# Optimization experiments

Measured on AMD Instinct MI355X. Metric: run time of the kernel, lower is better.

## Reference

```python
import jax, jax.numpy as jnp
import numpy as np

SEGMENT_LENGTHS = [2048, 4096, 8192]
DILATION_RATES = [1, 2, 4]
EPS = 1e-8


def setup_inputs() -> dict:
    key = jax.random.key(0)
    kq, kk, kv = jax.random.split(key, 3)
    shape = (4, 8192, 8, 64)  # (b, n, h, d)
    return {
        "query": jax.random.normal(kq, shape, dtype=jnp.float32),
        "key": jax.random.normal(kk, shape, dtype=jnp.float32),
        "value": jax.random.normal(kv, shape, dtype=jnp.float32),
    }


def _dilated_attention(query, key, value):
    b, n, h, d = query.shape
    ng = len(SEGMENT_LENGTHS)
    group_sizes = [h // ng] * ng
    for i in range(h % ng):
        group_sizes[i] += 1
    scale = 1.0 / (d ** 0.5)  # torch SDPA default: 1/sqrt(E), E = last dim

    out = jnp.zeros_like(query)
    for i, (g, r, s) in enumerate(zip(group_sizes, DILATION_RATES, SEGMENT_LENGTHS)):
        offset = i % r
        hmin = sum(group_sizes[:i])
        hmax = hmin + g
        nseg = n // s
        # (b, nseg, s, h, d) -> strided dilation slice + head-group slice
        qg = query.reshape(b, nseg, s, h, d)[:, :, offset::r, hmin:hmax, :]
        kg = key.reshape(b, nseg, s, h, d)[:, :, offset::r, hmin:hmax, :]
        vg = value.reshape(b, nseg, s, h, d)[:, :, offset::r, hmin:hmax, :]
        # Faithful to the torch code: SDPA is fed (bn, s, h, d) untransposed, so
        # attention is over the HEAD axis (length g); s is a batch-like axis.
        scores = jnp.einsum('bnsqd,bnskd->bnsqk', qg, kg) * scale  # (b,nseg,sd,g,g)
        attn = jax.nn.softmax(scores, axis=-1)
        x = jnp.einsum('bnsqk,bnskd->bnsqd', attn, vg)  # (b,nseg,sd,g,d)
        # custom sum-normalization over (segment, dilated-position) dims
        x = x / (x.sum(axis=(1, 2), keepdims=True) + EPS)
        # scatter-add back into the strided/head-sliced locations
        out = (out.reshape(b, nseg, s, h, d)
                  .at[:, :, offset::r, hmin:hmax, :].add(x)
                  .reshape(b, n, h, d))
    return out / ng


def reference(query, key, value):
    return _dilated_attention(query, key, value)
```

## Files before the change

### kernel.cpp

```cpp
#include <hip/hip_runtime.h>
#include <math.h>

#define NB 4
#define NN 8192
#define NH 8
#define ND 64
#define ROWF (NH * ND)
#define NPART_STRIDE 192
#define N_BLOCKS_P1 1792
#define N_WAVES_P1  (N_BLOCKS_P1 * 4)


__device__ __forceinline__ float dot4(float4 a, float4 b) {
    return a.x * b.x + a.y * b.y + a.z * b.z + a.w * b.w;
}

template<int HOFF>
__device__ __forceinline__ void pass1_g3(
    const float* __restrict__ Q, const float* __restrict__ K,
    const float* __restrict__ V, float* __restrict__ out,
    float* __restrict__ partials,
    int b, int cw, int wid, int r, int off, int seglen)
{
    const int lane = threadIdx.x & 63;
    const int sg   = lane >> 4;
    const int l15  = lane & 15;

    float xs0 = 0.f, xs1 = 0.f, xs2 = 0.f, xs3 = 0.f;

    #pragma unroll 2
    for (int t = 0; t < 8; ++t) {
        const int j   = cw * 8 + t;
        const int pos = (j >> 11) * seglen + off + (j & 2047) * r;
        const size_t rb = ((size_t)b * NN + pos) * ROWF;

        const float4 qv = *(const float4*)(Q + rb + HOFF + 4 * lane);
        const float4 k0 = *(const float4*)(K + rb + HOFF + 0 * ND + 4 * l15);
        const float4 k1 = *(const float4*)(K + rb + HOFF + 1 * ND + 4 * l15);
        const float4 k2 = *(const float4*)(K + rb + HOFF + 2 * ND + 4 * l15);
        const float4 v0 = *(const float4*)(V + rb + HOFF + 0 * ND + 4 * l15);
        const float4 v1 = *(const float4*)(V + rb + HOFF + 1 * ND + 4 * l15);
        const float4 v2 = *(const float4*)(V + rb + HOFF + 2 * ND + 4 * l15);

        float s0 = dot4(qv, k0), s1 = dot4(qv, k1), s2 = dot4(qv, k2);
        #pragma unroll
        for (int o = 8; o >= 1; o >>= 1) {
            s0 += __shfl_xor(s0, o);
            s1 += __shfl_xor(s1, o);
            s2 += __shfl_xor(s2, o);
        }

        s0 *= 0.125f; s1 *= 0.125f; s2 *= 0.125f;
        const float m  = fmaxf(s0, fmaxf(s1, s2));
        const float e0 = __expf(s0 - m), e1 = __expf(s1 - m), e2 = __expf(s2 - m);
        const float rs = 1.f / (e0 + e1 + e2);
        const float w0 = e0 * rs, w1 = e1 * rs, w2 = e2 * rs;

        const float xe0 = w0 * v0.x + w1 * v1.x + w2 * v2.x;
        const float xe1 = w0 * v0.y + w1 * v1.y + w2 * v2.y;
        const float xe2 = w0 * v0.z + w1 * v1.z + w2 * v2.z;
        const float xe3 = w0 * v0.w + w1 * v1.w + w2 * v2.w;

        if (sg < 3)
            *(float4*)(out + rb + HOFF + 4 * lane) = make_float4(xe0, xe1, xe2, xe3);
        xs0 += xe0; xs1 += xe1; xs2 += xe2; xs3 += xe3;
    }

    if (sg < 3)
        *(float4*)(partials + (size_t)wid * NPART_STRIDE + sg * 64 + 4 * l15) =
            make_float4(xs0, xs1, xs2, xs3);
}

__device__ __forceinline__ void pass1_g2(
    const float* __restrict__ Q, const float* __restrict__ K,
    const float* __restrict__ V, float* __restrict__ out,
    float* __restrict__ partials, int b, int cw, int wid)
{
    const int lane = threadIdx.x & 63;
    const int half = lane >> 5;
    const int sg2  = (lane >> 4) & 1;
    const int l15  = lane & 15;
    const int l31  = lane & 31;

    float xs0 = 0.f, xs1 = 0.f, xs2 = 0.f, xs3 = 0.f;

    #pragma unroll 2
    for (int t = 0; t < 4; ++t) {
        const int j   = cw * 8 + t * 2 + half;
        const int pos = 2 + 4 * j;
        const size_t rb = ((size_t)b * NN + pos) * ROWF + 384;

        const float4 qv = *(const float4*)(Q + rb + 4 * l31);
        const float4 k0 = *(const float4*)(K + rb + 0 * ND + 4 * l15);
        const float4 k1 = *(const float4*)(K + rb + 1 * ND + 4 * l15);
        const float4 v0 = *(const float4*)(V + rb + 0 * ND + 4 * l15);
        const float4 v1 = *(const float4*)(V + rb + 1 * ND + 4 * l15);

        float s0 = dot4(qv, k0), s1 = dot4(qv, k1);
        #pragma unroll
        for (int o = 8; o >= 1; o >>= 1) {
            s0 += __shfl_xor(s0, o);
            s1 += __shfl_xor(s1, o);
        }

        s0 *= 0.125f; s1 *= 0.125f;
        const float m  = fmaxf(s0, s1);
        const float e0 = __expf(s0 - m), e1 = __expf(s1 - m);
        const float rs = 1.f / (e0 + e1);
        const float w0 = e0 * rs, w1 = e1 * rs;

        const float xe0 = w0 * v0.x + w1 * v1.x;
        const float xe1 = w0 * v0.y + w1 * v1.y;
        const float xe2 = w0 * v0.z + w1 * v1.z;
        const float xe3 = w0 * v0.w + w1 * v1.w;

        *(float4*)(out + rb + 4 * l31) = make_float4(xe0, xe1, xe2, xe3);
        xs0 += xe0; xs1 += xe1; xs2 += xe2; xs3 += xe3;
    }

    xs0 += __shfl_xor(xs0, 32); xs1 += __shfl_xor(xs1, 32);
    xs2 += __shfl_xor(xs2, 32); xs3 += __shfl_xor(xs3, 32);
    if (half == 0)
        *(float4*)(partials + (size_t)wid * NPART_STRIDE + sg2 * 64 + 4 * l15) =
            make_float4(xs0, xs1, xs2, xs3);
}

__global__ __launch_bounds__(256)
void sda_pass1(const float* __restrict__ Q, const float* __restrict__ K,
               const float* __restrict__ V, float* __restrict__ out,
               float* __restrict__ partials)
{
    const int bid = blockIdx.x;
    const int w   = threadIdx.x >> 6;
    const int wid = bid * 4 + w;
    if (bid < 1024) {
        const int b = bid >> 8, cw = (bid & 255) * 4 + w;
        pass1_g3<0>(Q, K, V, out, partials, b, cw, wid, 1, 0, 2048);
    } else if (bid < 1536) {
        const int loc = bid - 1024;
        const int b = loc >> 7, cw = (loc & 127) * 4 + w;
        pass1_g3<192>(Q, K, V, out, partials, b, cw, wid, 2, 1, 4096);
    } else {
        const int loc = bid - 1536;
        const int b = loc >> 6, cw = (loc & 63) * 4 + w;
        pass1_g2(Q, K, V, out, partials, b, cw, wid);
    }
}

__global__ __launch_bounds__(256)
void sda_pass2a(const float* __restrict__ partials, float* __restrict__ partial2)
{
    const int bid   = blockIdx.x;
    const int bh    = bid >> 3;
    const int slice = bid & 7;
    const int b     = bh >> 3;
    const int h     = bh & 7;
    const int d     = threadIdx.x & 63;
    const int part  = threadIdx.x >> 6;
    int qi, wstart, cnt;
    if (h < 3)      { qi = h;     wstart = b * 1024;       cnt = 1024; }
    else if (h < 6) { qi = h - 3; wstart = 4096 + b * 512; cnt = 512;  }
    else            { qi = h - 6; wstart = 6144 + b * 256; cnt = 256;  }
    const int len = cnt >> 3;
    const int c0  = wstart + slice * len;
    float s = 0.f;
    #pragma unroll 4
    for (int c = part; c < len; c += 4)
        s += partials[(size_t)(c0 + c) * NPART_STRIDE + qi * 64 + d];
    __shared__ float sred[4][64];
    sred[part][d] = s;
    __syncthreads();
    if (part == 0)
        partial2[(size_t)bid * 64 + d] = sred[0][d] + sred[1][d] + sred[2][d] + sred[3][d];
}

__global__ __launch_bounds__(256)
void sda_pass2b(const float* __restrict__ partial2, float* __restrict__ inv)
{
    const int t = blockIdx.x * 256 + threadIdx.x;
    if (t >= NB * NH * ND) return;
    const int bh = t >> 6;
    const int d  = t & 63;
    float s = 0.f;
    #pragma unroll
    for (int sl = 0; sl < 8; ++sl)
        s += partial2[(size_t)(bh * 8 + sl) * 64 + d];
    inv[t] = 1.f / (3.f * (s + 1e-8f));
}

__global__ __launch_bounds__(256)
void sda_pass3(float* __restrict__ out, const float* __restrict__ inv)
{
    const int total4 = NB * NN * NH * ND / 4;
    for (int idx = blockIdx.x * 256 + threadIdx.x; idx < total4;
         idx += gridDim.x * 256) {
        const int d4  = idx & 15;
        const int rem = idx >> 4;
        const int h   = rem & 7;
        const int pos = (rem >> 3) & 8191;
        const int b   = rem >> 16;
        const bool cov = (h < 3) || ((h < 6) ? ((pos & 1) == 1) : ((pos & 3) == 2));
        float4 o;
        if (cov) {
            const float4 v = ((const float4*)out)[idx];
            const float4 f = ((const float4*)inv)[b * 128 + h * 16 + d4];
            o = make_float4(v.x * f.x, v.y * f.y, v.z * f.z, v.w * f.w);
        } else {
            o = make_float4(0.f, 0.f, 0.f, 0.f);
        }
        ((float4*)out)[idx] = o;
    }
}

extern "C" void kernel_launch(void* const* d_in, const int* in_sizes, int n_in,
                              void* d_out, int out_size, void* d_ws, size_t ws_size,
                              hipStream_t stream)
{
    const float* Q = (const float*)d_in[0];
    const float* K = (const float*)d_in[1];
    const float* V = (const float*)d_in[2];
    float* out      = (float*)d_out;
    float* partials = (float*)d_ws;
    float* partial2 = partials + (size_t)N_WAVES_P1 * NPART_STRIDE;
    float* inv      = partial2 + 256 * 64;

    hipLaunchKernelGGL(sda_pass1,  dim3(N_BLOCKS_P1), dim3(256), 0, stream,
                       Q, K, V, out, partials);
    hipLaunchKernelGGL(sda_pass2a, dim3(256), dim3(256), 0, stream, partials, partial2);
    hipLaunchKernelGGL(sda_pass2b, dim3(8),   dim3(256), 0, stream, partial2, inv);
    hipLaunchKernelGGL(sda_pass3,  dim3(2048), dim3(256), 0, stream, out, inv);
}
```

Baseline: 57.72 us.

## Process full rows per wave, computing all head groups with coalesced loads

Pass 1 now assigns each wave a run of consecutive positions and loads whole 512-float rows of Q, K and V with fully coalesced float4 loads. Per-head K and V slices are redistributed through lane shuffles, and the three head groups are computed according to position parity. Every output element, zero or not, is written in pass 1, so pass 3 becomes an unconditional scale. The aim is to replace strided, partially used loads and the three-way block split with contiguous traffic. In exchange, every position's row is read (the second half only skipped when pos%4==0), and the added shuffles and divergent branches cost extra ALU work.

```diff
diff --git a/kernel.cpp b/kernel.cpp
--- a/kernel.cpp
+++ b/kernel.cpp
@@ -5,146 +5,128 @@
 #define NN 8192
 #define NH 8
 #define ND 64
-#define ROWF (NH * ND)
-#define NPART_STRIDE 192
-#define N_BLOCKS_P1 1792
-#define N_WAVES_P1  (N_BLOCKS_P1 * 4)
-
+#define ROWF 512
+#define T_PER_WAVE 16
+#define N_BLOCKS_P1 512
+#define N_WAVES_P1 2048
+#define NPART 512
 
 __device__ __forceinline__ float dot4(float4 a, float4 b) {
     return a.x * b.x + a.y * b.y + a.z * b.z + a.w * b.w;
 }
-
-template<int HOFF>
-__device__ __forceinline__ void pass1_g3(
-    const float* __restrict__ Q, const float* __restrict__ K,
-    const float* __restrict__ V, float* __restrict__ out,
-    float* __restrict__ partials,
-    int b, int cw, int wid, int r, int off, int seglen)
-{
+__device__ __forceinline__ float4 shfl4(float4 v, int src) {
+    return make_float4(__shfl(v.x, src), __shfl(v.y, src),
+                       __shfl(v.z, src), __shfl(v.w, src));
+}
+__device__ __forceinline__ void bfly16(float& a) {
+    a += __shfl_xor(a, 8); a += __shfl_xor(a, 4);
+    a += __shfl_xor(a, 2); a += __shfl_xor(a, 1);
+}
+
+__global__ __launch_bounds__(256)
+void sda_pass1(const float* __restrict__ Q, const float* __restrict__ K,
+               const float* __restrict__ V, float* __restrict__ out,
+               float* __restrict__ partials)
+{
+    const int w    = threadIdx.x >> 6;
     const int lane = threadIdx.x & 63;
     const int sg   = lane >> 4;
     const int l15  = lane & 15;
-
-    float xs0 = 0.f, xs1 = 0.f, xs2 = 0.f, xs3 = 0.f;
-
-    #pragma unroll 2
-    for (int t = 0; t < 8; ++t) {
-        const int j   = cw * 8 + t;
-        const int pos = (j >> 11) * seglen + off + (j & 2047) * r;
+    const int wid  = blockIdx.x * 4 + w;
+    const int b    = wid >> 9;
+    const int j0   = (wid & 511) * T_PER_WAVE;
+
+    float4 xsA = make_float4(0.f, 0.f, 0.f, 0.f);
+    float4 xsB = make_float4(0.f, 0.f, 0.f, 0.f);
+
+    for (int t = 0; t < T_PER_WAVE; ++t) {
+        const int pos = j0 + t;
+        const int p4  = pos & 3;
         const size_t rb = ((size_t)b * NN + pos) * ROWF;
 
-        const float4 qv = *(const float4*)(Q + rb + HOFF + 4 * lane);
-        const float4 k0 = *(const float4*)(K + rb + HOFF + 0 * ND + 4 * l15);
-        const float4 k1 = *(const float4*)(K + rb + HOFF + 1 * ND + 4 * l15);
-        const float4 k2 = *(const float4*)(K + rb + HOFF + 2 * ND + 4 * l15);
-        const float4 v0 = *(const float4*)(V + rb + HOFF + 0 * ND + 4 * l15);
-        const float4 v1 = *(const float4*)(V + rb + HOFF + 1 * ND + 4 * l15);
-        const float4 v2 = *(const float4*)(V + rb + HOFF + 2 * ND + 4 * l15);
-
-        float s0 = dot4(qv, k0), s1 = dot4(qv, k1), s2 = dot4(qv, k2);
-        #pragma unroll
-        for (int o = 8; o >= 1; o >>= 1) {
-            s0 += __shfl_xor(s0, o);
-            s1 += __shfl_xor(s1, o);
-            s2 += __shfl_xor(s2, o);
-        }
-
-        s0 *= 0.125f; s1 *= 0.125f; s2 *= 0.125f;
-        const float m  = fmaxf(s0, fmaxf(s1, s2));
-        const float e0 = __expf(s0 - m), e1 = __expf(s1 - m), e2 = __expf(s2 - m);
-        const float rs = 1.f / (e0 + e1 + e2);
-        const float w0 = e0 * rs, w1 = e1 * rs, w2 = e2 * rs;
-
-        const float xe0 = w0 * v0.x + w1 * v1.x + w2 * v2.x;
-        const float xe1 = w0 * v0.y + w1 * v1.y + w2 * v2.y;
-        const float xe2 = w0 * v0.z + w1 * v1.z + w2 * v2.z;
-        const float xe3 = w0 * v0.w + w1 * v1.w + w2 * v2.w;
-
-        if (sg < 3)
-            *(float4*)(out + rb + HOFF + 4 * lane) = make_float4(xe0, xe1, xe2, xe3);
-        xs0 += xe0; xs1 += xe1; xs2 += xe2; xs3 += xe3;
+        const float4 qA = *(const float4*)(Q + rb + 4 * lane);
+        const float4 kA = *(const float4*)(K + rb + 4 * lane);
+        const float4 vA = *(const float4*)(V + rb + 4 * lane);
+        float4 qB, kB, vB;
+        if (p4 != 0) {
+            qB = *(const float4*)(Q + rb + 256 + 4 * lane);
+            kB = *(const float4*)(K + rb + 256 + 4 * lane);
+            vB = *(const float4*)(V + rb + 256 + 4 * lane);
+        } else {
+            qB = kB = vB = make_float4(0.f, 0.f, 0.f, 0.f);
+        }
+
+        float4 aA = make_float4(0.f, 0.f, 0.f, 0.f);
+        float4 aB = make_float4(0.f, 0.f, 0.f, 0.f);
+
+        {
+            const float4 K0 = shfl4(kA, l15), K1 = shfl4(kA, 16 + l15),
+                         K2 = shfl4(kA, 32 + l15);
+            float m0 = dot4(qA, K0), m1 = dot4(qA, K1), m2 = dot4(qA, K2);
+            bfly16(m0); bfly16(m1); bfly16(m2);
+            m0 *= 0.125f; m1 *= 0.125f; m2 *= 0.125f;
+            const float mm = fmaxf(m0, fmaxf(m1, m2));
+            const float e0 = __expf(m0 - mm), e1 = __expf(m1 - mm), e2 = __expf(m2 - mm);
+            const float rs = 1.f / (e0 + e1 + e2);
+            const float w0 = e0 * rs, w1 = e1 * rs, w2 = e2 * rs;
+            const float4 V0 = shfl4(vA, l15), V1 = shfl4(vA, 16 + l15),
+                         V2 = shfl4(vA, 32 + l15);
+            float4 x;
+            x.x = w0 * V0.x + w1 * V1.x + w2 * V2.x;
+            x.y = w0 * V0.y + w1 * V1.y + w2 * V2.y;
+            x.z = w0 * V0.z + w1 * V1.z + w2 * V2.z;
+            x.w = w0 * V0.w + w1 * V1.w + w2 * V2.w;
+            if (sg < 3) aA = x;
+        }
+
+        if (pos & 1) {
+            const float4 K3 = shfl4(kA, 48 + l15), K4 = shfl4(kB, l15),
+                         K5 = shfl4(kB, 16 + l15);
+            const float4 qg = (sg == 3) ? qA : qB;
+            float m3 = dot4(qg, K3), m4 = dot4(qg, K4), m5 = dot4(qg, K5);
+            bfly16(m3); bfly16(m4); bfly16(m5);
+            m3 *= 0.125f; m4 *= 0.125f; m5 *= 0.125f;
+            const float mm = fmaxf(m3, fmaxf(m4, m5));
+            const float e3 = __expf(m3 - mm), e4 = __expf(m4 - mm), e5 = __expf(m5 - mm);
+            const float rs = 1.f / (e3 + e4 + e5);
+            const float w3 = e3 * rs, w4 = e4 * rs, w5 = e5 * rs;
+            const float4 V3 = shfl4(vA, 48 + l15), V4 = shfl4(vB, l15),
+                         V5 = shfl4(vB, 16 + l15);
+            float4 x;
+            x.x = w3 * V3.x + w4 * V4.x + w5 * V5.x;
+            x.y = w3 * V3.y + w4 * V4.y + w5 * V5.y;
+            x.z = w3 * V3.z + w4 * V4.z + w5 * V5.z;
+            x.w = w3 * V3.w + w4 * V4.w + w5 * V5.w;
+            if (sg == 3) aA = x;
+            if (sg < 2)  aB = x;
+        }
+
+        if (p4 == 2) {
+            const float4 K6 = shfl4(kB, 32 + l15), K7 = shfl4(kB, 48 + l15);
+            float m6 = dot4(qB, K6), m7 = dot4(qB, K7);
+            bfly16(m6); bfly16(m7);
+            m6 *= 0.125f; m7 *= 0.125f;
+            const float mm = fmaxf(m6, m7);
+            const float e6 = __expf(m6 - mm), e7 = __expf(m7 - mm);
+            const float rs = 1.f / (e6 + e7);
+            const float w6 = e6 * rs, w7 = e7 * rs;
+            const float4 V6 = shfl4(vB, 32 + l15), V7 = shfl4(vB, 48 + l15);
+            float4 x;
+            x.x = w6 * V6.x + w7 * V7.x;
+            x.y = w6 * V6.y + w7 * V7.y;
+            x.z = w6 * V6.z + w7 * V7.z;
+            x.w = w6 * V6.w + w7 * V7.w;
+            if (sg >= 2) aB = x;
+        }
+
+        *(float4*)(out + rb + 4 * lane)       = aA;
+        *(float4*)(out + rb + 256 + 4 * lane) = aB;
+        xsA.x += aA.x; xsA.y += aA.y; xsA.z += aA.z; xsA.w += aA.w;
+        xsB.x += aB.x; xsB.y += aB.y; xsB.z += aB.z; xsB.w += aB.w;
     }
 
-    if (sg < 3)
-        *(float4*)(partials + (size_t)wid * NPART_STRIDE + sg * 64 + 4 * l15) =
-            make_float4(xs0, xs1, xs2, xs3);
-}
-
-__device__ __forceinline__ void pass1_g2(
-    const float* __restrict__ Q, const float* __restrict__ K,
-    const float* __restrict__ V, float* __restrict__ out,
-    float* __restrict__ partials, int b, int cw, int wid)
-{
-    const int lane = threadIdx.x & 63;
-    const int half = lane >> 5;
-    const int sg2  = (lane >> 4) & 1;
-    const int l15  = lane & 15;
-    const int l31  = lane & 31;
-
-    float xs0 = 0.f, xs1 = 0.f, xs2 = 0.f, xs3 = 0.f;
-
-    #pragma unroll 2
-    for (int t = 0; t < 4; ++t) {
-        const int j   = cw * 8 + t * 2 + half;
-        const int pos = 2 + 4 * j;
-        const size_t rb = ((size_t)b * NN + pos) * ROWF + 384;
-
-        const float4 qv = *(const float4*)(Q + rb + 4 * l31);
-        const float4 k0 = *(const float4*)(K + rb + 0 * ND + 4 * l15);
-        const float4 k1 = *(const float4*)(K + rb + 1 * ND + 4 * l15);
-        const float4 v0 = *(const float4*)(V + rb + 0 * ND + 4 * l15);
-        const float4 v1 = *(const float4*)(V + rb + 1 * ND + 4 * l15);
-
-        float s0 = dot4(qv, k0), s1 = dot4(qv, k1);
-        #pragma unroll
-        for (int o = 8; o >= 1; o >>= 1) {
-            s0 += __shfl_xor(s0, o);
-            s1 += __shfl_xor(s1, o);
-        }
-
-        s0 *= 0.125f; s1 *= 0.125f;
-        const float m  = fmaxf(s0, s1);
-        const float e0 = __expf(s0 - m), e1 = __expf(s1 - m);
-        const float rs = 1.f / (e0 + e1);
-        const float w0 = e0 * rs, w1 = e1 * rs;
-
-        const float xe0 = w0 * v0.x + w1 * v1.x;
-        const float xe1 = w0 * v0.y + w1 * v1.y;
-        const float xe2 = w0 * v0.z + w1 * v1.z;
-        const float xe3 = w0 * v0.w + w1 * v1.w;
-
-        *(float4*)(out + rb + 4 * l31) = make_float4(xe0, xe1, xe2, xe3);
-        xs0 += xe0; xs1 += xe1; xs2 += xe2; xs3 += xe3;
-    }
-
-    xs0 += __shfl_xor(xs0, 32); xs1 += __shfl_xor(xs1, 32);
-    xs2 += __shfl_xor(xs2, 32); xs3 += __shfl_xor(xs3, 32);
-    if (half == 0)
-        *(float4*)(partials + (size_t)wid * NPART_STRIDE + sg2 * 64 + 4 * l15) =
-            make_float4(xs0, xs1, xs2, xs3);
-}
-
-__global__ __launch_bounds__(256)
-void sda_pass1(const float* __restrict__ Q, const float* __restrict__ K,
-               const float* __restrict__ V, float* __restrict__ out,
-               float* __restrict__ partials)
-{
-    const int bid = blockIdx.x;
-    const int w   = threadIdx.x >> 6;
-    const int wid = bid * 4 + w;
-    if (bid < 1024) {
-        const int b = bid >> 8, cw = (bid & 255) * 4 + w;
-        pass1_g3<0>(Q, K, V, out, partials, b, cw, wid, 1, 0, 2048);
-    } else if (bid < 1536) {
-        const int loc = bid - 1024;
-        const int b = loc >> 7, cw = (loc & 127) * 4 + w;
-        pass1_g3<192>(Q, K, V, out, partials, b, cw, wid, 2, 1, 4096);
-    } else {
-        const int loc = bid - 1536;
-        const int b = loc >> 6, cw = (loc & 63) * 4 + w;
-        pass1_g2(Q, K, V, out, partials, b, cw, wid);
-    }
+    *(float4*)(partials + (size_t)wid * NPART + sg * 64 + 4 * l15)       = xsA;
+    *(float4*)(partials + (size_t)wid * NPART + (4 + sg) * 64 + 4 * l15) = xsB;
 }
 
 __global__ __launch_bounds__(256)
@@ -157,16 +139,11 @@
     const int h     = bh & 7;
     const int d     = threadIdx.x & 63;
     const int part  = threadIdx.x >> 6;
-    int qi, wstart, cnt;
-    if (h < 3)      { qi = h;     wstart = b * 1024;       cnt = 1024; }
-    else if (h < 6) { qi = h - 3; wstart = 4096 + b * 512; cnt = 512;  }
-    else            { qi = h - 6; wstart = 6144 + b * 256; cnt = 256;  }
-    const int len = cnt >> 3;
-    const int c0  = wstart + slice * len;
+    const int w0    = b * 512 + slice * 64;
     float s = 0.f;
     #pragma unroll 4
-    for (int c = part; c < len; c += 4)
-        s += partials[(size_t)(c0 + c) * NPART_STRIDE + qi * 64 + d];
+    for (int c = part; c < 64; c += 4)
+        s += partials[(size_t)(w0 + c) * NPART + h * 64 + d];
     __shared__ float sred[4][64];
     sred[part][d] = s;
     __syncthreads();
@@ -194,21 +171,12 @@
     const int total4 = NB * NN * NH * ND / 4;
     for (int idx = blockIdx.x * 256 + threadIdx.x; idx < total4;
          idx += gridDim.x * 256) {
-        const int d4  = idx & 15;
-        const int rem = idx >> 4;
-        const int h   = rem & 7;
-        const int pos = (rem >> 3) & 8191;
-        const int b   = rem >> 16;
-        const bool cov = (h < 3) || ((h < 6) ? ((pos & 1) == 1) : ((pos & 3) == 2));
-        float4 o;
-        if (cov) {
-            const float4 v = ((const float4*)out)[idx];
-            const float4 f = ((const float4*)inv)[b * 128 + h * 16 + d4];
-            o = make_float4(v.x * f.x, v.y * f.y, v.z * f.z, v.w * f.w);
-        } else {
-            o = make_float4(0.f, 0.f, 0.f, 0.f);
-        }
-        ((float4*)out)[idx] = o;
+        const int d4 = idx & 15;
+        const int h  = (idx >> 4) & 7;
+        const int b  = idx >> 20;
+        const float4 v = ((const float4*)out)[idx];
+        const float4 f = ((const float4*)inv)[(b * 8 + h) * 16 + d4];
+        ((float4*)out)[idx] = make_float4(v.x * f.x, v.y * f.y, v.z * f.z, v.w * f.w);
     }
 }
 
@@ -221,7 +189,7 @@
     const float* V = (const float*)d_in[2];
     float* out      = (float*)d_out;
     float* partials = (float*)d_ws;
-    float* partial2 = partials + (size_t)N_WAVES_P1 * NPART_STRIDE;
+    float* partial2 = partials + (size_t)N_WAVES_P1 * NPART;
     float* inv      = partial2 + 256 * 64;
 
     hipLaunchKernelGGL(sda_pass1,  dim3(N_BLOCKS_P1), dim3(256), 0, stream,
```

Result: slower. 67.65 us (+17.2%).
